# Kernel tuning notes

Measured on AMD Instinct MI355X. Metric: run time of the kernel, lower is better.

## Reference

```python
import jax, jax.numpy as jnp
import numpy as np

B, N, M, HW = 8, 256, 32, 32768
W_CLASS, W_CENTER, W_MASK, W_DICE = 2.0, 1.0, 5.0, 2.0


def setup_inputs() -> dict:
    key = jax.random.key(0)
    ks = jax.random.split(key, 6)
    sem_cls_prob = jax.random.uniform(ks[0], (B, N, 1), dtype=jnp.float32)
    center_dist = jax.random.uniform(ks[1], (B, N, M), dtype=jnp.float32)
    mask_heatmaps = jax.random.normal(ks[2], (B, HW, N), dtype=jnp.float32)
    # binary targets, as assumed by the dice/BCE cost math
    mask_tgt = jnp.round(jax.random.uniform(ks[3], (B, M, HW), dtype=jnp.float32))
    gt_plane_sem_cls_label = jax.random.randint(ks[4], (B, M), 0, 2).astype(jnp.int64)
    nactual_gt = jax.random.randint(ks[5], (B,), 1, M + 1).astype(jnp.int64)
    return {
        'sem_cls_prob': sem_cls_prob,
        'center_dist': center_dist,
        'mask_heatmaps': mask_heatmaps,
        'mask_tgt': mask_tgt,
        'gt_plane_sem_cls_label': gt_plane_sem_cls_label,
        'nactual_gt': nactual_gt,
    }


def _final_cost(sem_cls_prob, center_dist, mask_heatmaps, mask_tgt, labels):
    # class cost: -gathered prob from cat(1-p, p) -> [B, N, M]
    cls_cat = jnp.concatenate([1.0 - sem_cls_prob, sem_cls_prob], axis=-1)  # [B, N, 2]
    lbl = jnp.broadcast_to(labels[:, None, :], (B, N, M))
    class_mat = -jnp.take_along_axis(cls_cat, lbl, axis=2)

    x = jnp.swapaxes(mask_heatmaps, 1, 2)  # [B, N, HW] logits (mask_heatmaps[b].T)
    # BCE-with-logits: pos = softplus(-x) (target=1), neg = x + softplus(-x) (target=0)
    pos = jax.nn.softplus(-x)
    neg = x + pos
    cost_mask = (jnp.einsum('bnc,bmc->bnm', pos, mask_tgt)
                 + jnp.einsum('bnc,bmc->bnm', neg, 1.0 - mask_tgt)) / HW

    s = jax.nn.sigmoid(x)
    numerator = 2.0 * jnp.einsum('bnc,bmc->bnm', s, mask_tgt)
    denominator = s.sum(-1)[:, :, None] + mask_tgt.sum(-1)[:, None, :]
    cost_dice = 1.0 - (numerator + 1.0) / (denominator + 1.0)

    return (W_CLASS * class_mat + W_CENTER * center_dist
            + W_MASK * cost_mask + W_DICE * cost_dice)


def reference(sem_cls_prob, center_dist, mask_heatmaps, mask_tgt,
              gt_plane_sem_cls_label, nactual_gt):
    # nactual_gt only gates the (serial, CPU) Hungarian step, which is out of
    # kernel scope; the GPU-side math is the fused final cost matrix.
    return _final_cost(sem_cls_prob, center_dist, mask_heatmaps, mask_tgt,
                       gt_plane_sem_cls_label)
```

## Files before the change

kernel.cpp:

```cpp
#include <hip/hip_runtime.h>
#include <hip/hip_bf16.h>

#define NB   8
#define NN   256
#define NM   32
#define NHW  32768

#define CCH    64
#define CSLAB  (NHW / CCH)
#define KC     32
#define KSTEPS (CSLAB / KC)

#define OFF_DXP  0
#define SZ_DXP   (CCH*NB*NN*NM)
#define OFF_DSP  (OFF_DXP + SZ_DXP)
#define OFF_SNP  (OFF_DSP + SZ_DXP)
#define SZ_SNP   (CCH*NB*NN)
#define OFF_SSP  (OFF_SNP + SZ_SNP)
#define OFF_STGT (OFF_SSP + SZ_SNP)

typedef _Float16 half8 __attribute__((ext_vector_type(8)));
typedef float    f32x4 __attribute__((ext_vector_type(4)));

#define MFMA16(a, b, c) __builtin_amdgcn_mfma_f32_16x16x32_f16(a, b, c, 0, 0, 0)

typedef const __attribute__((address_space(1))) unsigned int* gp_t;
typedef __attribute__((address_space(3))) unsigned int*       lp_t;

__device__ __forceinline__ void stage_row(const float* gsrc, float* ldst, int lane) {
#if __has_builtin(__builtin_amdgcn_global_load_lds)
    __builtin_amdgcn_global_load_lds((gp_t)(const void*)(gsrc + lane * 4),
                                     (lp_t)(void*)ldst, 16, 0, 0);
#else
    float4 v = *(const float4*)(gsrc + lane * 4);
    *(float4*)(ldst + lane * 4) = v;
#endif
}

__global__ __launch_bounds__(512, 4) void cost_main(
    const float* __restrict__ X,
    const float* __restrict__ T,
    float* __restrict__ ws) {
    const int blk = blockIdx.x;
    const int b   = blk & 7;
    const int ch  = blk >> 3;

    const int tid  = threadIdx.x;
    const int wave = tid >> 6;
    const int lane = tid & 63;
    const int l16  = lane & 15;
    const int quad = lane >> 4;

    const int c0 = ch * CSLAB;

    __shared__ __align__(16) float xs[2][KC][NN];

    const float* Xbase = X + ((size_t)b * NHW + c0) * NN;
    const float* Tp0   = T + ((size_t)b * NM + l16) * NHW + c0 + quad * 8;
    const float* Tp1   = Tp0 + (size_t)16 * NHW;

#pragma unroll
    for (int r = 0; r < 4; ++r) {
        const int row = wave + r * 8;
        stage_row(Xbase + (size_t)row * NN, &xs[0][row][0], lane);
    }

    f32x4 ax0[2], ax1[2], as0[2], as1[2];
#pragma unroll
    for (int f = 0; f < 2; ++f) {
        ax0[f] = f32x4{0.f, 0.f, 0.f, 0.f};
        ax1[f] = f32x4{0.f, 0.f, 0.f, 0.f};
        as0[f] = f32x4{0.f, 0.f, 0.f, 0.f};
        as1[f] = f32x4{0.f, 0.f, 0.f, 0.f};
    }
    float sneg[2] = {0.f, 0.f};
    float ssig[2] = {0.f, 0.f};
    float ts0 = 0.f, ts1 = 0.f;

    for (int ks = 0; ks < KSTEPS; ++ks) {
        __syncthreads();
        const int nb = ks + 1;
        if (nb < KSTEPS) {
            const float* Xn = Xbase + (size_t)nb * KC * NN;
#pragma unroll
            for (int r = 0; r < 4; ++r) {
                const int row = wave + r * 8;
                stage_row(Xn + (size_t)row * NN, &xs[nb & 1][row][0], lane);
            }
        }

        float4 ta = *(const float4*)(Tp0 + ks * KC);
        float4 tb = *(const float4*)(Tp0 + ks * KC + 4);
        float4 tc = *(const float4*)(Tp1 + ks * KC);
        float4 td = *(const float4*)(Tp1 + ks * KC + 4);
        half8 ht0 = {(_Float16)ta.x, (_Float16)ta.y, (_Float16)ta.z, (_Float16)ta.w,
                     (_Float16)tb.x, (_Float16)tb.y, (_Float16)tb.z, (_Float16)tb.w};
        half8 ht1 = {(_Float16)tc.x, (_Float16)tc.y, (_Float16)tc.z, (_Float16)tc.w,
                     (_Float16)td.x, (_Float16)td.y, (_Float16)td.z, (_Float16)td.w};
        ts0 += (ta.x + ta.y) + (ta.z + ta.w) + (tb.x + tb.y) + (tb.z + tb.w);
        ts1 += (tc.x + tc.y) + (tc.z + tc.w) + (td.x + td.y) + (td.z + td.w);

#pragma unroll
        for (int f = 0; f < 2; ++f) {
            const int n = wave * 32 + f * 16 + l16;
            float xv[8];
#pragma unroll
            for (int j = 0; j < 8; ++j)
                xv[j] = xs[ks & 1][quad * 8 + j][n];
            half8 hx, hs;
#pragma unroll
            for (int j = 0; j < 8; ++j) {
                float x = xv[j];
                float e = __expf(-fabsf(x));
                float rc = __builtin_amdgcn_rcpf(1.f + e);
                float s  = (x >= 0.f) ? rc : 1.f - rc;
                float pos = fmaxf(-x, 0.f) + __logf(1.f + e);
                sneg[f] += x + pos;
                ssig[f] += s;
                hx[j] = (_Float16)x;
                hs[j] = (_Float16)s;
            }
            ax0[f] = MFMA16(hx, ht0, ax0[f]);
            ax1[f] = MFMA16(hx, ht1, ax1[f]);
            as0[f] = MFMA16(hs, ht0, as0[f]);
            as1[f] = MFMA16(hs, ht1, as1[f]);
        }
    }

#pragma unroll
    for (int f = 0; f < 2; ++f) {
        float sn = sneg[f], ss = ssig[f];
        sn += __shfl_xor(sn, 16); sn += __shfl_xor(sn, 32);
        ss += __shfl_xor(ss, 16); ss += __shfl_xor(ss, 32);
        if (lane < 16) {
            const size_t sb = ((size_t)ch * NB + b) * NN + wave * 32 + f * 16 + l16;
            ws[OFF_SNP + sb] = sn;
            ws[OFF_SSP + sb] = ss;
        }
    }
    if (wave == 0) {
        float t0 = ts0, t1 = ts1;
        t0 += __shfl_xor(t0, 16); t0 += __shfl_xor(t0, 32);
        t1 += __shfl_xor(t1, 16); t1 += __shfl_xor(t1, 32);
        if (lane < 16) {
            const size_t tb_ = ((size_t)ch * NB + b) * NM;
            ws[OFF_STGT + tb_ + l16]      = t0;
            ws[OFF_STGT + tb_ + l16 + 16] = t1;
        }
    }
    const size_t dbase = ((size_t)ch * NB + b) * NN * NM;
#pragma unroll
    for (int f = 0; f < 2; ++f) {
#pragma unroll
        for (int r = 0; r < 4; ++r) {
            const int n = wave * 32 + f * 16 + quad * 4 + r;
            const size_t o = dbase + (size_t)n * NM;
            ws[OFF_DXP + o + l16]      = ax0[f][r];
            ws[OFF_DXP + o + l16 + 16] = ax1[f][r];
            ws[OFF_DSP + o + l16]      = as0[f][r];
            ws[OFF_DSP + o + l16 + 16] = as1[f][r];
        }
    }
}

__global__ __launch_bounds__(256) void cost_finalize(
    const float* __restrict__ P,
    const float* __restrict__ CD,
    const int*   __restrict__ LAB,
    const float* __restrict__ ws,
    float* __restrict__ out) {
    const int idx = blockIdx.x * 256 + threadIdx.x;
    const int m = idx & 31;
    const int n = (idx >> 5) & 255;
    const int b = idx >> 13;

    float dx = 0.f, ds = 0.f, sn = 0.f, ss = 0.f, st = 0.f;
    for (int ch = 0; ch < CCH; ++ch) {
        const size_t e = (size_t)ch * NB + b;
        dx += ws[OFF_DXP + (e * NN + n) * NM + m];
        ds += ws[OFF_DSP + (e * NN + n) * NM + m];
        sn += ws[OFF_SNP + e * NN + n];
        ss += ws[OFF_SSP + e * NN + n];
        st += ws[OFF_STGT + e * NM + m];
    }
    const float p   = P[b * NN + n];
    const int   lab = LAB[b * NM + m];
    const float cls = lab ? -p : (p - 1.f);

    const float cmask = (sn - dx) * (1.f / (float)NHW);
    const float dice  = 1.f - (2.f * ds + 1.f) / (ss + st + 1.f);

    out[idx] = 2.f * cls + CD[idx] + 5.f * cmask + 2.f * dice;
}

extern "C" void kernel_launch(void* const* d_in, const int* in_sizes, int n_in,
                              void* d_out, int out_size, void* d_ws, size_t ws_size,
                              hipStream_t stream) {
    const float* P   = (const float*)d_in[0];
    const float* CD  = (const float*)d_in[1];
    const float* X   = (const float*)d_in[2];
    const float* T   = (const float*)d_in[3];
    const int*   LAB = (const int*)d_in[4];
    float* out = (float*)d_out;
    float* ws  = (float*)d_ws;

    hipLaunchKernelGGL(cost_main, dim3(NB * CCH), dim3(512), 0, stream, X, T, ws);
    hipLaunchKernelGGL(cost_finalize, dim3((NB * NN * NM) / 256), dim3(256), 0, stream,
                       P, CD, LAB, ws, out);
}
```

Measured before the change: 419.8 us.

## Rotate LDS staging to avoid bank conflicts and parallelize finalize reduction across chunks

Each staged row of X is rotated by a per-row offset when written into LDS. The read columns are remapped so that the 8 row reads in each quad hit different banks, which is meant to cut LDS bank conflicts in the main kernel. The finalize kernel now uses one block per (b,n). Its 8 thread groups each sum 8 of the 64 channel partials, then combine through shared memory, which spreads the serial 64-step reduction across more threads. This adds a __syncthreads and leaves only 32 of 256 threads active for the final write.

```diff
diff --git a/kernel.cpp b/kernel.cpp
--- a/kernel.cpp
+++ b/kernel.cpp
@@ -27,12 +27,14 @@
 typedef const __attribute__((address_space(1))) unsigned int* gp_t;
 typedef __attribute__((address_space(3))) unsigned int*       lp_t;
 
-__device__ __forceinline__ void stage_row(const float* gsrc, float* ldst, int lane) {
+__device__ __forceinline__ void stage_row(const float* gsrc, float* ldst,
+                                          int lane, int rot) {
+    const int src = ((lane << 2) - rot) & 255;
 #if __has_builtin(__builtin_amdgcn_global_load_lds)
-    __builtin_amdgcn_global_load_lds((gp_t)(const void*)(gsrc + lane * 4),
+    __builtin_amdgcn_global_load_lds((gp_t)(const void*)(gsrc + src),
                                      (lp_t)(void*)ldst, 16, 0, 0);
 #else
-    float4 v = *(const float4*)(gsrc + lane * 4);
+    float4 v = *(const float4*)(gsrc + src);
     *(float4*)(ldst + lane * 4) = v;
 #endif
 }
@@ -59,10 +61,13 @@
     const float* Tp0   = T + ((size_t)b * NM + l16) * NHW + c0 + quad * 8;
     const float* Tp1   = Tp0 + (size_t)16 * NHW;
 
+    const int col0 = ((wave << 5) + l16 + (quad << 3)) & 255;
+    const int col1 = (col0 + 16) & 255;
+
 #pragma unroll
     for (int r = 0; r < 4; ++r) {
         const int row = wave + r * 8;
-        stage_row(Xbase + (size_t)row * NN, &xs[0][row][0], lane);
+        stage_row(Xbase + (size_t)row * NN, &xs[0][row][0], lane, r << 3);
     }
 
     f32x4 ax0[2], ax1[2], as0[2], as1[2];
@@ -85,7 +90,7 @@
 #pragma unroll
             for (int r = 0; r < 4; ++r) {
                 const int row = wave + r * 8;
-                stage_row(Xn + (size_t)row * NN, &xs[nb & 1][row][0], lane);
+                stage_row(Xn + (size_t)row * NN, &xs[nb & 1][row][0], lane, r << 3);
             }
         }
 
@@ -102,11 +107,11 @@
 
 #pragma unroll
         for (int f = 0; f < 2; ++f) {
-            const int n = wave * 32 + f * 16 + l16;
+            const int colf = f ? col1 : col0;
             float xv[8];
 #pragma unroll
             for (int j = 0; j < 8; ++j)
-                xv[j] = xs[ks & 1][quad * 8 + j][n];
+                xv[j] = xs[ks & 1][quad * 8 + j][colf];
             half8 hx, hs;
 #pragma unroll
             for (int j = 0; j < 8; ++j) {
@@ -169,28 +174,48 @@
     const int*   __restrict__ LAB,
     const float* __restrict__ ws,
     float* __restrict__ out) {
-    const int idx = blockIdx.x * 256 + threadIdx.x;
-    const int m = idx & 31;
-    const int n = (idx >> 5) & 255;
-    const int b = idx >> 13;
+    const int bn = blockIdx.x;
+    const int n  = bn & 255;
+    const int b  = bn >> 8;
+    const int t  = threadIdx.x;
+    const int m  = t & 31;
+    const int q  = t >> 5;
 
     float dx = 0.f, ds = 0.f, sn = 0.f, ss = 0.f, st = 0.f;
-    for (int ch = 0; ch < CCH; ++ch) {
+#pragma unroll
+    for (int k = 0; k < 8; ++k) {
+        const int ch = q * 8 + k;
         const size_t e = (size_t)ch * NB + b;
-        dx += ws[OFF_DXP + (e * NN + n) * NM + m];
-        ds += ws[OFF_DSP + (e * NN + n) * NM + m];
+        const size_t o = (e * NN + n) * NM + m;
+        dx += ws[OFF_DXP + o];
+        ds += ws[OFF_DSP + o];
         sn += ws[OFF_SNP + e * NN + n];
         ss += ws[OFF_SSP + e * NN + n];
         st += ws[OFF_STGT + e * NM + m];
     }
-    const float p   = P[b * NN + n];
-    const int   lab = LAB[b * NM + m];
-    const float cls = lab ? -p : (p - 1.f);
-
-    const float cmask = (sn - dx) * (1.f / (float)NHW);
-    const float dice  = 1.f - (2.f * ds + 1.f) / (ss + st + 1.f);
-
-    out[idx] = 2.f * cls + CD[idx] + 5.f * cmask + 2.f * dice;
+
+    __shared__ float red[5][8][32];
+    red[0][q][m] = dx; red[1][q][m] = ds; red[2][q][m] = sn;
+    red[3][q][m] = ss; red[4][q][m] = st;
+    __syncthreads();
+
+    if (t < 32) {
+        float a0 = 0.f, a1 = 0.f, a2 = 0.f, a3 = 0.f, a4 = 0.f;
+#pragma unroll
+        for (int k = 0; k < 8; ++k) {
+            a0 += red[0][k][m]; a1 += red[1][k][m]; a2 += red[2][k][m];
+            a3 += red[3][k][m]; a4 += red[4][k][m];
+        }
+        const float p   = P[bn];
+        const int   lab = LAB[b * NM + m];
+        const float cls = lab ? -p : (p - 1.f);
+
+        const float cmask = (a2 - a0) * (1.f / (float)NHW);
+        const float dice  = 1.f - (2.f * a1 + 1.f) / (a3 + a4 + 1.f);
+
+        const size_t o = (size_t)bn * NM + m;
+        out[o] = 2.f * cls + CD[o] + 5.f * cmask + 2.f * dice;
+    }
 }
 
 extern "C" void kernel_launch(void* const* d_in, const int* in_sizes, int n_in,
@@ -205,6 +230,6 @@
     float* ws  = (float*)d_ws;
 
     hipLaunchKernelGGL(cost_main, dim3(NB * CCH), dim3(512), 0, stream, X, T, ws);
-    hipLaunchKernelGGL(cost_finalize, dim3((NB * NN * NM) / 256), dim3(256), 0, stream,
+    hipLaunchKernelGGL(cost_finalize, dim3(NB * NN), dim3(256), 0, stream,
                        P, CD, LAB, ws, out);
 }
```

After: 420.8 us. Within noise of the previous version (+0.3%).
